# Kernel optimization log

Hardware: AMD Instinct MI355X
Metric: run time of the kernel (lower is better)

Reference implementation:

```python
import jax, jax.numpy as jnp
import numpy as np


def setup_inputs() -> dict:
    key = jax.random.key(0)
    ks = jax.random.split(key, 11)
    B, H, P, D, E = 64, 20, 448, 64, 1280
    s = 0.02
    return {
        "hidden_states": jax.random.normal(ks[0], (B, 1, E), jnp.float32),
        "past_k": jax.random.normal(ks[1], (B, H, P, D), jnp.float32),
        "past_v": jax.random.normal(ks[2], (B, H, P, D), jnp.float32),
        "past_keep_mask": jnp.zeros((1, 1, 1, P), jnp.float32),
        "Wq": jax.random.normal(ks[3], (E, E), jnp.float32) * s,
        "bq": jax.random.normal(ks[4], (E,), jnp.float32) * s,
        "Wk": jax.random.normal(ks[5], (E, E), jnp.float32) * s,
        "Wv": jax.random.normal(ks[6], (E, E), jnp.float32) * s,
        "bv": jax.random.normal(ks[7], (E,), jnp.float32) * s,
        "Wo": jax.random.normal(ks[8], (E, E), jnp.float32) * s,
        "bo": jax.random.normal(ks[9], (E,), jnp.float32) * s,
    }


def reference(hidden_states, past_k, past_v, past_keep_mask, Wq, bq, Wk, Wv, bv, Wo, bo):
    B, S, E = hidden_states.shape  # S == 1 (decode step)
    H, D = past_k.shape[1], past_k.shape[3]
    scale = jnp.asarray(D, jnp.float32) ** -0.5

    def split_heads(x):  # [B,S,E] -> [B,H,S,D]
        return x.reshape(B, S, H, D).transpose(0, 2, 1, 3)

    q = split_heads((hidden_states @ Wq.T + bq) * scale)
    new_k = split_heads(hidden_states @ Wk.T)
    new_v = split_heads(hidden_states @ Wv.T + bv)

    all_k = jnp.concatenate([past_k, new_k], axis=2)  # [B,H,P+1,D]
    all_v = jnp.concatenate([past_v, new_v], axis=2)
    mask = jnp.concatenate(
        [past_keep_mask, jnp.zeros((1, 1, 1, 1), past_keep_mask.dtype)], axis=-1
    )  # [1,1,1,P+1]

    attn = jnp.einsum("bhqd,bhkd->bhqk", q, all_k) + mask
    attn = jax.nn.softmax(attn, axis=-1)
    ctx = jnp.einsum("bhqk,bhkd->bhqd", attn, all_v)  # [B,H,S,D]
    merged = ctx.transpose(0, 2, 1, 3).reshape(B, S, E)
    out = merged @ Wo.T + bo
    return out, new_k, new_v
```

## Files before the change

kernel.cpp:

```cpp
#include <hip/hip_runtime.h>

#define EDIM 1280
#define BDIM 64
#define HDIM 20
#define PDIM 448
#define DDIM 64
#define NCOL 3840
#define NCHUNK 4
#define ECHUNK 320
#define CTILE 32
#define KCHUNKS 7

__device__ __forceinline__ float dot4(float4 a, float4 b) {
    return a.x * b.x + a.y * b.y + a.z * b.z + a.w * b.w;
}

template <int AUX>
__device__ __forceinline__ void dma16(const float* g, float* l) {
    __builtin_amdgcn_global_load_lds(
        (const __attribute__((address_space(1))) void*)(g),
        (__attribute__((address_space(3))) void*)(l),
        16, 0, AUX);
}

template <int AUX>
__device__ __forceinline__ void dma_tile(const float* tbase, float* lbase,
                                         int w, int lane) {
#pragma unroll
    for (int r = 0; r < 4; ++r) {
        dma16<AUX>(tbase + (size_t)(r * 256 + w * 64 + lane) * 4,
                   lbase + (r * 256 + w * 64) * 4);
    }
}

__global__ __launch_bounds__(256) void proj_qkv(
    const float* __restrict__ h,
    const float* __restrict__ Wq, const float* __restrict__ Wk,
    const float* __restrict__ Wv,
    float* __restrict__ partial)
{
    __shared__ float Wt[CTILE * ECHUNK];

    const int wave = threadIdx.x >> 6;
    const int lane = threadIdx.x & 63;
    const int colbase = blockIdx.x * CTILE;
    const int e0 = blockIdx.y * ECHUNK;

    const float* W; int wc;
    if (colbase < EDIM)          { W = Wq; wc = colbase; }
    else if (colbase < 2 * EDIM) { W = Wk; wc = colbase - EDIM; }
    else                         { W = Wv; wc = colbase - 2 * EDIM; }

#pragma unroll
    for (int i = 0; i < 10; ++i) {
        int i4 = (i * 256 + threadIdx.x) * 4;
        int c  = i4 / ECHUNK;
        int e  = i4 - c * ECHUNK;
        *reinterpret_cast<float4*>(&Wt[i4]) =
            *reinterpret_cast<const float4*>(&W[(size_t)(wc + c) * EDIM + e0 + e]);
    }
    __syncthreads();

    float acc[8];
#pragma unroll
    for (int c = 0; c < 8; ++c) acc[c] = 0.f;

    const float4* hp = reinterpret_cast<const float4*>(h + lane * EDIM + e0);
    const int c0 = wave * 8;
#pragma unroll 4
    for (int eg = 0; eg < ECHUNK / 4; ++eg) {
        float4 hv = hp[eg];
#pragma unroll
        for (int c = 0; c < 8; ++c) {
            float4 wv = *reinterpret_cast<const float4*>(&Wt[(c0 + c) * ECHUNK + eg * 4]);
            acc[c] += dot4(hv, wv);
        }
    }
#pragma unroll
    for (int c = 0; c < 8; ++c)
        partial[((size_t)blockIdx.y * NCOL + colbase + c0 + c) * 64 + lane] = acc[c];
}

__global__ __launch_bounds__(256) void reduce_proj(
    const float* __restrict__ partial,
    const float* __restrict__ bq, const float* __restrict__ bv,
    float* __restrict__ qout, float* __restrict__ kout, float* __restrict__ vout)
{
    __shared__ float tile[256];
    const int cg0 = blockIdx.x * 4;
    const int idx = cg0 * 64 + threadIdx.x;
    float v = partial[idx] + partial[245760 + idx]
            + partial[491520 + idx] + partial[737280 + idx];
    tile[threadIdx.x] = v;
    __syncthreads();
    const int row = threadIdx.x >> 2;
    const int c   = threadIdx.x & 3;
    const int cg  = cg0 + c;
    const float v2 = tile[c * 64 + row];
    if (cg < EDIM)
        qout[row * EDIM + cg] = (v2 + bq[cg]) * 0.125f;
    else if (cg < 2 * EDIM)
        kout[row * EDIM + (cg - EDIM)] = v2;
    else
        vout[row * EDIM + (cg - 2 * EDIM)] = v2 + bv[cg - 2 * EDIM];
}

__global__ __launch_bounds__(256) void attn_part(
    const float* __restrict__ q,
    const float* __restrict__ Kpast,
    const float* __restrict__ Vpast,
    const float* __restrict__ mask,
    float* __restrict__ ctxbuf,
    float* __restrict__ msbuf)
{
    __shared__ __align__(16) float kbuf[4096];
    __shared__ __align__(16) float vbuf[4096];

    const int chunk = blockIdx.x;
    const int bh    = blockIdx.y;
    const int b  = bh / HDIM;
    const int hh = bh % HDIM;
    const int t  = threadIdx.x;
    const int w  = t >> 6;
    const int lane = t & 63;
    const int grp = t >> 4;
    const int dg  = t & 15;

    const float* Kt = Kpast + ((size_t)bh * PDIM + chunk * 64) * DDIM;
    const float* Vt = Vpast + ((size_t)bh * PDIM + chunk * 64) * DDIM;

    dma_tile<2>(Kt, kbuf, w, lane);
    dma_tile<0>(Vt, vbuf, w, lane);

    const int j0 = chunk * 64 + grp;
    const float4 qv = *reinterpret_cast<const float4*>(q + b * EDIM + hh * DDIM + dg * 4);
    const float mk0 = mask[j0], mk1 = mask[j0 + 16];
    const float mk2 = mask[j0 + 32], mk3 = mask[j0 + 48];

    __syncthreads();

    float4 k0 = *reinterpret_cast<const float4*>(kbuf + grp * DDIM + dg * 4);
    float4 k1 = *reinterpret_cast<const float4*>(kbuf + (grp + 16) * DDIM + dg * 4);
    float4 k2 = *reinterpret_cast<const float4*>(kbuf + (grp + 32) * DDIM + dg * 4);
    float4 k3 = *reinterpret_cast<const float4*>(kbuf + (grp + 48) * DDIM + dg * 4);
    float s0 = dot4(qv, k0), s1 = dot4(qv, k1), s2 = dot4(qv, k2), s3 = dot4(qv, k3);
#pragma unroll
    for (int off = 8; off; off >>= 1) {
        s0 += __shfl_xor(s0, off, 16);
        s1 += __shfl_xor(s1, off, 16);
        s2 += __shfl_xor(s2, off, 16);
        s3 += __shfl_xor(s3, off, 16);
    }
    s0 += mk0; s1 += mk1; s2 += mk2; s3 += mk3;

    float m4 = fmaxf(fmaxf(s0, s1), fmaxf(s2, s3));
    m4 = fmaxf(m4, __shfl_xor(m4, 16, 64));
    m4 = fmaxf(m4, __shfl_xor(m4, 32, 64));

    __syncthreads();
    float* redm = kbuf;
    float* reds = kbuf + 8;
    float4* ctxp = reinterpret_cast<float4*>(kbuf + 16);

    if (lane == 0) redm[w] = m4;
    __syncthreads();
    const float mx = fmaxf(fmaxf(redm[0], redm[1]), fmaxf(redm[2], redm[3]));

    float p0 = __expf(s0 - mx), p1 = __expf(s1 - mx);
    float p2 = __expf(s2 - mx), p3 = __expf(s3 - mx);
    float ls = p0 + p1 + p2 + p3;
    ls += __shfl_xor(ls, 16, 64);
    ls += __shfl_xor(ls, 32, 64);

    float4 v0 = *reinterpret_cast<const float4*>(vbuf + grp * DDIM + dg * 4);
    float4 v1 = *reinterpret_cast<const float4*>(vbuf + (grp + 16) * DDIM + dg * 4);
    float4 v2 = *reinterpret_cast<const float4*>(vbuf + (grp + 32) * DDIM + dg * 4);
    float4 v3 = *reinterpret_cast<const float4*>(vbuf + (grp + 48) * DDIM + dg * 4);

    float4 acc;
    acc.x = p0 * v0.x + p1 * v1.x + p2 * v2.x + p3 * v3.x;
    acc.y = p0 * v0.y + p1 * v1.y + p2 * v2.y + p3 * v3.y;
    acc.z = p0 * v0.z + p1 * v1.z + p2 * v2.z + p3 * v3.z;
    acc.w = p0 * v0.w + p1 * v1.w + p2 * v2.w + p3 * v3.w;
    acc.x += __shfl_xor(acc.x, 16, 64); acc.y += __shfl_xor(acc.y, 16, 64);
    acc.z += __shfl_xor(acc.z, 16, 64); acc.w += __shfl_xor(acc.w, 16, 64);
    acc.x += __shfl_xor(acc.x, 32, 64); acc.y += __shfl_xor(acc.y, 32, 64);
    acc.z += __shfl_xor(acc.z, 32, 64); acc.w += __shfl_xor(acc.w, 32, 64);

    if (lane == 0) reds[w] = ls;
    if (lane < 16) ctxp[w * 16 + lane] = acc;
    __syncthreads();

    if (t < 16) {
        float4 a0 = ctxp[t], a1 = ctxp[16 + t], a2 = ctxp[32 + t], a3 = ctxp[48 + t];
        float4 r;
        r.x = a0.x + a1.x + a2.x + a3.x;
        r.y = a0.y + a1.y + a2.y + a3.y;
        r.z = a0.z + a1.z + a2.z + a3.z;
        r.w = a0.w + a1.w + a2.w + a3.w;
        *reinterpret_cast<float4*>(ctxbuf + ((size_t)bh * KCHUNKS + chunk) * 64 + t * 4) = r;
    }
    if (t == 0) {
        msbuf[((size_t)bh * KCHUNKS + chunk) * 2 + 0] = mx;
        msbuf[((size_t)bh * KCHUNKS + chunk) * 2 + 1] = reds[0] + reds[1] + reds[2] + reds[3];
    }
}

__global__ __launch_bounds__(256) void attn_combine(
    const float* __restrict__ q,
    const float* __restrict__ knew,
    const float* __restrict__ vnew,
    const float* __restrict__ ctxbuf,
    const float* __restrict__ msbuf,
    float* __restrict__ merged)
{
    const int unit = blockIdx.x * 4 + (threadIdx.x >> 6);
    const int lane = threadIdx.x & 63;
    const int b  = unit / HDIM;
    const int hh = unit % HDIM;

    float mc[KCHUNKS], sc[KCHUNKS];
    float M = -3.4e38f;
#pragma unroll
    for (int c = 0; c < KCHUNKS; ++c) {
        mc[c] = msbuf[((size_t)unit * KCHUNKS + c) * 2 + 0];
        sc[c] = msbuf[((size_t)unit * KCHUNKS + c) * 2 + 1];
        M = fmaxf(M, mc[c]);
    }

    const int base = b * EDIM + hh * DDIM + lane;
    float sn = q[base] * knew[base];
#pragma unroll
    for (int off = 32; off; off >>= 1) sn += __shfl_xor(sn, off, 64);

    const float M2 = fmaxf(M, sn);
    const float pn = __expf(sn - M2);
    float S   = pn;
    float ctx = pn * vnew[base];
#pragma unroll
    for (int c = 0; c < KCHUNKS; ++c) {
        float e = __expf(mc[c] - M2);
        S   += sc[c] * e;
        ctx += e * ctxbuf[((size_t)unit * KCHUNKS + c) * 64 + lane];
    }
    merged[base] = ctx / S;
}

__global__ __launch_bounds__(256) void proj_out(
    const float* __restrict__ x,
    const float* __restrict__ Wo,
    float* __restrict__ partial)
{
    __shared__ float Wt[CTILE * ECHUNK];

    const int wave = threadIdx.x >> 6;
    const int lane = threadIdx.x & 63;
    const int colbase = blockIdx.x * CTILE;
    const int e0 = blockIdx.y * ECHUNK;

#pragma unroll
    for (int i = 0; i < 10; ++i) {
        int i4 = (i * 256 + threadIdx.x) * 4;
        int c  = i4 / ECHUNK;
        int e  = i4 - c * ECHUNK;
        *reinterpret_cast<float4*>(&Wt[i4]) =
            *reinterpret_cast<const float4*>(&Wo[(size_t)(colbase + c) * EDIM + e0 + e]);
    }
    __syncthreads();

    float acc[8];
#pragma unroll
    for (int c = 0; c < 8; ++c) acc[c] = 0.f;

    const float4* xp = reinterpret_cast<const float4*>(x + lane * EDIM + e0);
    const int c0 = wave * 8;
#pragma unroll 4
    for (int eg = 0; eg < ECHUNK / 4; ++eg) {
        float4 hv = xp[eg];
#pragma unroll
        for (int c = 0; c < 8; ++c) {
            float4 wv = *reinterpret_cast<const float4*>(&Wt[(c0 + c) * ECHUNK + eg * 4]);
            acc[c] += dot4(hv, wv);
        }
    }
#pragma unroll
    for (int c = 0; c < 8; ++c)
        partial[((size_t)blockIdx.y * EDIM + colbase + c0 + c) * 64 + lane] = acc[c];
}

__global__ __launch_bounds__(256) void reduce_out(
    const float* __restrict__ partial, const float* __restrict__ bo,
    float* __restrict__ out)
{
    __shared__ float tile[256];
    const int cg0 = blockIdx.x * 4;
    const int idx = cg0 * 64 + threadIdx.x;
    float v = partial[idx] + partial[81920 + idx]
            + partial[163840 + idx] + partial[245760 + idx];
    tile[threadIdx.x] = v;
    __syncthreads();
    const int row = threadIdx.x >> 2;
    const int c   = threadIdx.x & 3;
    const int cg  = cg0 + c;
    out[row * EDIM + cg] = tile[c * 64 + row] + bo[cg];
}

extern "C" void kernel_launch(void* const* d_in, const int* in_sizes, int n_in,
                              void* d_out, int out_size, void* d_ws, size_t ws_size,
                              hipStream_t stream)
{
    const float* h    = (const float*)d_in[0];
    const float* pk   = (const float*)d_in[1];
    const float* pv   = (const float*)d_in[2];
    const float* mask = (const float*)d_in[3];
    const float* Wq   = (const float*)d_in[4];
    const float* bq   = (const float*)d_in[5];
    const float* Wk   = (const float*)d_in[6];
    const float* Wv   = (const float*)d_in[7];
    const float* bv   = (const float*)d_in[8];
    const float* Wo   = (const float*)d_in[9];
    const float* bo   = (const float*)d_in[10];

    float* out  = (float*)d_out;
    float* kout = (float*)d_out + 81920;
    float* vout = (float*)d_out + 163840;

    float* ws    = (float*)d_ws;
    float* partP = ws;
    float* ctxb  = ws;
    float* msb   = ws + 573440;
    float* qbuf  = ws + 983040;
    float* mrg   = ws + 983040 + 81920;
    float* partO = ws + 983040 + 163840;

    proj_qkv<<<dim3(NCOL / CTILE, NCHUNK), 256, 0, stream>>>(h, Wq, Wk, Wv, partP);
    reduce_proj<<<dim3(NCOL / 4), 256, 0, stream>>>(partP, bq, bv, qbuf, kout, vout);
    attn_part<<<dim3(KCHUNKS, BDIM * HDIM), 256, 0, stream>>>(qbuf, pk, pv, mask, ctxb, msb);
    attn_combine<<<dim3(BDIM * HDIM / 4), 256, 0, stream>>>(qbuf, kout, vout, ctxb, msb, mrg);
    proj_out<<<dim3(EDIM / CTILE, NCHUNK), 256, 0, stream>>>(mrg, Wo, partO);
    reduce_out<<<dim3(EDIM / 4), 256, 0, stream>>>(partO, bo, out);
}
```

Before: 98.03 us.

## Split attention chunk kernel into separate score and PV kernels

Result: slower. 101.4 us (+3.4%).

```diff
diff --git a/kernel.cpp b/kernel.cpp
--- a/kernel.cpp
+++ b/kernel.cpp
@@ -105,16 +105,14 @@
         vout[row * EDIM + (cg - 2 * EDIM)] = v2 + bv[cg - 2 * EDIM];
 }
 
-__global__ __launch_bounds__(256) void attn_part(
+__global__ __launch_bounds__(256) void attn_score(
     const float* __restrict__ q,
     const float* __restrict__ Kpast,
-    const float* __restrict__ Vpast,
     const float* __restrict__ mask,
-    float* __restrict__ ctxbuf,
+    float* __restrict__ pbuf,
     float* __restrict__ msbuf)
 {
     __shared__ __align__(16) float kbuf[4096];
-    __shared__ __align__(16) float vbuf[4096];
 
     const int chunk = blockIdx.x;
     const int bh    = blockIdx.y;
@@ -127,10 +125,8 @@
     const int dg  = t & 15;
 
     const float* Kt = Kpast + ((size_t)bh * PDIM + chunk * 64) * DDIM;
-    const float* Vt = Vpast + ((size_t)bh * PDIM + chunk * 64) * DDIM;
 
     dma_tile<2>(Kt, kbuf, w, lane);
-    dma_tile<0>(Vt, vbuf, w, lane);
 
     const int j0 = chunk * 64 + grp;
     const float4 qv = *reinterpret_cast<const float4*>(q + b * EDIM + hh * DDIM + dg * 4);
@@ -160,17 +156,57 @@
     __syncthreads();
     float* redm = kbuf;
     float* reds = kbuf + 8;
-    float4* ctxp = reinterpret_cast<float4*>(kbuf + 16);
 
     if (lane == 0) redm[w] = m4;
     __syncthreads();
     const float mx = fmaxf(fmaxf(redm[0], redm[1]), fmaxf(redm[2], redm[3]));
 
-    float p0 = __expf(s0 - mx), p1 = __expf(s1 - mx);
-    float p2 = __expf(s2 - mx), p3 = __expf(s3 - mx);
+    const float p0 = __expf(s0 - mx), p1 = __expf(s1 - mx);
+    const float p2 = __expf(s2 - mx), p3 = __expf(s3 - mx);
     float ls = p0 + p1 + p2 + p3;
     ls += __shfl_xor(ls, 16, 64);
     ls += __shfl_xor(ls, 32, 64);
+    if (lane == 0) reds[w] = ls;
+
+    const size_t pb = ((size_t)bh * KCHUNKS + chunk) * 64;
+    if (dg == 0) {
+        pbuf[pb + grp]      = p0;
+        pbuf[pb + grp + 16] = p1;
+        pbuf[pb + grp + 32] = p2;
+        pbuf[pb + grp + 48] = p3;
+    }
+    __syncthreads();
+    if (t == 0) {
+        msbuf[((size_t)bh * KCHUNKS + chunk) * 2 + 0] = mx;
+        msbuf[((size_t)bh * KCHUNKS + chunk) * 2 + 1] = reds[0] + reds[1] + reds[2] + reds[3];
+    }
+}
+
+__global__ __launch_bounds__(256) void attn_pv(
+    const float* __restrict__ Vpast,
+    const float* __restrict__ pbuf,
+    float* __restrict__ ctxbuf)
+{
+    __shared__ __align__(16) float vbuf[4096];
+
+    const int chunk = blockIdx.x;
+    const int bh    = blockIdx.y;
+    const int t  = threadIdx.x;
+    const int w  = t >> 6;
+    const int lane = t & 63;
+    const int grp = t >> 4;
+    const int dg  = t & 15;
+
+    const float* Vt = Vpast + ((size_t)bh * PDIM + chunk * 64) * DDIM;
+    dma_tile<0>(Vt, vbuf, w, lane);
+
+    const size_t pb = ((size_t)bh * KCHUNKS + chunk) * 64;
+    const float p0 = pbuf[pb + grp];
+    const float p1 = pbuf[pb + grp + 16];
+    const float p2 = pbuf[pb + grp + 32];
+    const float p3 = pbuf[pb + grp + 48];
+
+    __syncthreads();
 
     float4 v0 = *reinterpret_cast<const float4*>(vbuf + grp * DDIM + dg * 4);
     float4 v1 = *reinterpret_cast<const float4*>(vbuf + (grp + 16) * DDIM + dg * 4);
@@ -187,7 +223,8 @@
     acc.x += __shfl_xor(acc.x, 32, 64); acc.y += __shfl_xor(acc.y, 32, 64);
     acc.z += __shfl_xor(acc.z, 32, 64); acc.w += __shfl_xor(acc.w, 32, 64);
 
-    if (lane == 0) reds[w] = ls;
+    __syncthreads();
+    float4* ctxp = reinterpret_cast<float4*>(vbuf);
     if (lane < 16) ctxp[w * 16 + lane] = acc;
     __syncthreads();
 
@@ -199,10 +236,6 @@
         r.z = a0.z + a1.z + a2.z + a3.z;
         r.w = a0.w + a1.w + a2.w + a3.w;
         *reinterpret_cast<float4*>(ctxbuf + ((size_t)bh * KCHUNKS + chunk) * 64 + t * 4) = r;
-    }
-    if (t == 0) {
-        msbuf[((size_t)bh * KCHUNKS + chunk) * 2 + 0] = mx;
-        msbuf[((size_t)bh * KCHUNKS + chunk) * 2 + 1] = reds[0] + reds[1] + reds[2] + reds[3];
     }
 }
 
@@ -329,13 +362,15 @@
     float* partP = ws;
     float* ctxb  = ws;
     float* msb   = ws + 573440;
-    float* qbuf  = ws + 983040;
-    float* mrg   = ws + 983040 + 81920;
-    float* partO = ws + 983040 + 163840;
+    float* pbuf  = ws + 591360;
+    float* partO = ws + 591360;
+    float* qbuf  = ws + 1164800;
+    float* mrg   = ws + 1246720;
 
     proj_qkv<<<dim3(NCOL / CTILE, NCHUNK), 256, 0, stream>>>(h, Wq, Wk, Wv, partP);
     reduce_proj<<<dim3(NCOL / 4), 256, 0, stream>>>(partP, bq, bv, qbuf, kout, vout);
-    attn_part<<<dim3(KCHUNKS, BDIM * HDIM), 256, 0, stream>>>(qbuf, pk, pv, mask, ctxb, msb);
+    attn_score<<<dim3(KCHUNKS, BDIM * HDIM), 256, 0, stream>>>(qbuf, pk, mask, pbuf, msb);
+    attn_pv<<<dim3(KCHUNKS, BDIM * HDIM), 256, 0, stream>>>(pv, pbuf, ctxb);
     attn_combine<<<dim3(BDIM * HDIM / 4), 256, 0, stream>>>(qbuf, kout, vout, ctxb, msb, mrg);
     proj_out<<<dim3(EDIM / CTILE, NCHUNK), 256, 0, stream>>>(mrg, Wo, partO);
     reduce_out<<<dim3(EDIM / 4), 256, 0, stream>>>(partO, bo, out);
```
